# Performance work log

Hardware: AMD Instinct MI355X
Metric: run time of the kernel (lower is better)

Reference implementation:

```python
import jax, jax.numpy as jnp
import numpy as np

HIDDEN = 4096
N_HEADS = 32
N_KV_HEADS = 8
HEAD_DIM = 128
ROPE_THETA = 1000000.0
EPS = 1e-06
B, T = 1, 2048


def apply_rope(inputs, position_ids, head_dim, theta):
    # inputs: [B, T, H, D], position_ids: [B, T]
    fraction = 2 * jnp.arange(0, head_dim // 2, dtype=jnp.float32) / head_dim
    timescale = jnp.power(theta, fraction)  # [D/2]
    x = (position_ids.astype(jnp.float32)[..., None] / timescale[None, None, :])[..., None, :]  # [B,T,1,D/2]
    sin, cos = jnp.sin(x), jnp.cos(x)
    a, b = jnp.split(inputs, 2, axis=-1)
    return jnp.concatenate([a * cos - b * sin, b * cos + a * sin], axis=-1).astype(inputs.dtype)


def rms_norm(x, weight, eps=EPS):
    rms = jnp.sqrt(jnp.mean(x * x, axis=-1, keepdims=True) + eps)
    return weight * x / rms


def setup_inputs() -> dict:
    key = jax.random.key(0)
    ks = jax.random.split(key, 8)
    lecun = lambda k, shape: jax.random.normal(k, shape, jnp.float32) / np.sqrt(shape[0])
    return {
        "x": jax.random.normal(ks[0], (B, T, HIDDEN), jnp.float32),
        "Wq": lecun(ks[1], (HIDDEN, N_HEADS * HEAD_DIM)),
        "Wk": lecun(ks[2], (HIDDEN, N_KV_HEADS * HEAD_DIM)),
        "Wv": lecun(ks[3], (HIDDEN, N_KV_HEADS * HEAD_DIM)),
        "Wo": lecun(ks[4], (N_HEADS * HEAD_DIM, HIDDEN)),
        "q_norm_w": 1.0 + 0.01 * jax.random.normal(ks[5], (HEAD_DIM,), jnp.float32),
        "k_norm_w": 1.0 + 0.01 * jax.random.normal(ks[6], (HEAD_DIM,), jnp.float32),
        "attention_mask": jnp.ones((B, T), jnp.int32),
        "positions": jnp.broadcast_to(jnp.arange(T, dtype=jnp.int32)[None, :], (B, T)),
    }


def reference(x, Wq, Wk, Wv, Wo, q_norm_w, k_norm_w, attention_mask, positions):
    b, t, _ = x.shape
    q = rms_norm((x @ Wq).reshape(b, t, N_HEADS, HEAD_DIM), q_norm_w)
    k = rms_norm((x @ Wk).reshape(b, t, N_KV_HEADS, HEAD_DIM), k_norm_w)
    v = (x @ Wv).reshape(b, t, N_KV_HEADS, HEAD_DIM)
    q = apply_rope(q, positions, HEAD_DIM, ROPE_THETA)
    k = apply_rope(k, positions, HEAD_DIM, ROPE_THETA)
    # prefill path: kv_cache is None -> causal attention, padding mask on keys
    attn = jax.nn.dot_product_attention(
        q, k, v,
        scale=1.0 / HEAD_DIM ** 0.5,
        mask=attention_mask[:, None, None, :].astype(bool),
        is_causal=True,
    )
    out = attn.reshape(b, t, N_HEADS * HEAD_DIM) @ Wo
    return out, (k, v)
```

## Files before the change

kernel.cpp:

```cpp
#include <hip/hip_runtime.h>


typedef __bf16 bf16;
typedef __bf16 bf16x8 __attribute__((ext_vector_type(8)));
typedef float  f32x4  __attribute__((ext_vector_type(4)));

#define MFMA16(a, b, c) __builtin_amdgcn_mfma_f32_16x16x32_bf16((a), (b), (c), 0, 0, 0)

__device__ __forceinline__ void gll16(const void* g, void* l) {
    __builtin_amdgcn_global_load_lds(
        (const __attribute__((address_space(1))) void*)g,
        (__attribute__((address_space(3))) void*)l,
        16, 0, 0);
}

__global__ __launch_bounds__(256) void detect_convert(
    const unsigned short* __restrict__ probe,
    const void* __restrict__ qw_raw, const void* __restrict__ kw_raw,
    int* __restrict__ flag, bf16* __restrict__ qwc, bf16* __restrict__ kwc) {
    __shared__ int cnt;
    if (threadIdx.x == 0) cnt = 0;
    __syncthreads();
    int local = 0;
    for (int i = 0; i < 4; ++i) {
        const unsigned short w = probe[(threadIdx.x * 4 + i) * 2];
        const int e = (w >> 7) & 0xFF;
        if (e >= 90 && e <= 140) ++local;
    }
    atomicAdd(&cnt, local);
    __syncthreads();
    const bool isbf16 = cnt >= 700;
    if (threadIdx.x == 0) *flag = isbf16 ? 1 : 0;
    const int t = threadIdx.x;
    if (t < 128)
        qwc[t] = isbf16 ? ((const bf16*)qw_raw)[t] : (bf16)((const float*)qw_raw)[t];
    else
        kwc[t - 128] = isbf16 ? ((const bf16*)kw_raw)[t - 128] : (bf16)((const float*)kw_raw)[t - 128];
}

__global__ __launch_bounds__(256) void convert_x(const void* __restrict__ xv,
                                                 bf16* __restrict__ xb,
                                                 const int* __restrict__ flag) {
    const size_t i8 = ((size_t)blockIdx.x * 256 + threadIdx.x) * 8;
    if (*flag) {
        *(bf16x8*)&xb[i8] = *(const bf16x8*)&((const bf16*)xv)[i8];
    } else {
        const f32x4 a = *(const f32x4*)&((const float*)xv)[i8];
        const f32x4 b = *(const f32x4*)&((const float*)xv)[i8 + 4];
        bf16x8 o;
#pragma unroll
        for (int e = 0; e < 4; ++e) { o[e] = (bf16)a[e]; o[e + 4] = (bf16)b[e]; }
        *(bf16x8*)&xb[i8] = o;
    }
}

__global__ __launch_bounds__(256) void transpose_w(
    const void* __restrict__ Wq, const void* __restrict__ Wk, const void* __restrict__ Wv,
    bf16* __restrict__ WqT, bf16* __restrict__ WkT, bf16* __restrict__ WvT,
    const int* __restrict__ flag) {
    __shared__ float T[64][65];
    int id = blockIdx.x;
    const void* src;
    bf16* dst;
    int N, tn, tk;
    if (id < 4096) {
        src = Wq; dst = WqT; N = 4096; tn = id & 63; tk = id >> 6;
    } else {
        id -= 4096;
        if (id < 1024) { src = Wk; dst = WkT; }
        else           { src = Wv; dst = WvT; id -= 1024; }
        N = 1024; tn = id & 15; tk = id >> 4;
    }
    const int k0 = tk * 64, n0 = tn * 64;
    const bool bB = (*flag) != 0;
    const int tx = threadIdx.x & 63, ty = threadIdx.x >> 6;
#pragma unroll
    for (int p = 0; p < 16; ++p) {
        const int k = ty + p * 4;
        T[k][tx] = bB ? (float)((const bf16*)src)[(size_t)(k0 + k) * N + n0 + tx]
                      : ((const float*)src)[(size_t)(k0 + k) * N + n0 + tx];
    }
    __syncthreads();
#pragma unroll
    for (int p = 0; p < 16; ++p) {
        const int n = ty + p * 4;
        dst[(size_t)(n0 + n) * 4096 + k0 + tx] = (bf16)T[tx][n];
    }
}

__global__ __launch_bounds__(256) void gemm_bt(
    const bf16* __restrict__ A,
    const bf16* __restrict__ B1T, const bf16* __restrict__ B2T,
    bf16* __restrict__ C1, bf16* __restrict__ C2,
    int K, int ldc1, int ldc2, int ns1) {
    __shared__ __align__(16) bf16 As[128 * 64];
    __shared__ __align__(16) bf16 Bs[128 * 64];

    const int nbxp = (int)gridDim.x >> 3;
    int id = blockIdx.y * gridDim.x + blockIdx.x;
    const int xcd = id & 7;
    const int j = id >> 3;
    const int bx = xcd * nbxp + j / (int)gridDim.y;
    const int by = j % (int)gridDim.y;

    const bf16* BT;
    bf16* C;
    int n0, ldc;
    if (bx < ns1) { BT = B1T; C = C1; n0 = bx * 128; ldc = ldc1; }
    else          { BT = B2T; C = C2; n0 = (bx - ns1) * 128; ldc = ldc2; }
    const int m0 = by * 128;

    const int tid  = threadIdx.x;
    const int wave = tid >> 6;
    const int lane = tid & 63;
    const int l15  = lane & 15;
    const int quad = lane >> 4;
    const int axor = l15 & 7;
    const int wm = (wave >> 1) * 64;
    const int wn = (wave & 1) * 64;
    const int l8 = lane >> 3;

    const bf16* aP = A  + (size_t)(m0 + wave * 8 + l8) * K + (((lane & 7) ^ l8) << 3);
    const bf16* bP = BT + (size_t)(n0 + wave * 8 + l8) * K + (((lane & 7) ^ l8) << 3);

    f32x4 acc[4][4];
#pragma unroll
    for (int i = 0; i < 4; ++i)
#pragma unroll
        for (int j2 = 0; j2 < 4; ++j2) acc[i][j2] = {0.f, 0.f, 0.f, 0.f};

    const int nt = K >> 6;
    for (int t = 0; t < nt; ++t) {
        const int k0 = t << 6;
#pragma unroll
        for (int p = 0; p < 4; ++p)
            gll16(aP + (size_t)p * 32 * K + k0, &As[p * 2048 + wave * 512]);
#pragma unroll
        for (int p = 0; p < 4; ++p)
            gll16(bP + (size_t)p * 32 * K + k0, &Bs[p * 2048 + wave * 512]);
        __syncthreads();
#pragma unroll
        for (int kk = 0; kk < 64; kk += 32) {
            bf16x8 af[4], bfr[4];
#pragma unroll
            for (int i = 0; i < 4; ++i)
                af[i] = *(const bf16x8*)&As[(wm + i * 16 + l15) * 64 +
                        (((kk >> 3) + quad) ^ axor) * 8];
#pragma unroll
            for (int j3 = 0; j3 < 4; ++j3)
                bfr[j3] = *(const bf16x8*)&Bs[(wn + j3 * 16 + l15) * 64 +
                          (((kk >> 3) + quad) ^ axor) * 8];
#pragma unroll
            for (int i = 0; i < 4; ++i)
#pragma unroll
                for (int j3 = 0; j3 < 4; ++j3)
                    acc[i][j3] = MFMA16(af[i], bfr[j3], acc[i][j3]);
        }
        __syncthreads();
    }

#pragma unroll
    for (int i = 0; i < 4; ++i)
#pragma unroll
        for (int j2 = 0; j2 < 4; ++j2)
#pragma unroll
            for (int r = 0; r < 4; ++r) {
                const int row = m0 + wm + i * 16 + quad * 4 + r;
                const int col = n0 + wn + j2 * 16 + l15;
                C[(size_t)row * ldc + col] = (bf16)acc[i][j2][r];
            }
}

#define GBM 128
#define GBN 128
#define GBK 64
#define GLD 72

__global__ __launch_bounds__(256) void gemm_nt(
    const bf16* __restrict__ A,
    const void* __restrict__ B1v, const void* __restrict__ B2v, const void* __restrict__ B3v,
    bf16* __restrict__ Cb1, float* __restrict__ Cf1,
    bf16* __restrict__ Cb2, float* __restrict__ Cf2,
    bf16* __restrict__ Cb3, float* __restrict__ Cf3,
    const int* __restrict__ flag, int K,
    int ldb1, int ldb2, int ldb3, int ldc1, int ldc2, int ldc3,
    int ns1, int ns2) {
    __shared__ __align__(16) bf16 As[2][GBM * 64];
    __shared__ __align__(16) bf16 Bs[GBN * GLD];

    const int nbxp = (int)gridDim.x >> 3;
    int id = blockIdx.y * gridDim.x + blockIdx.x;
    const int xcd = id & 7;
    const int j = id >> 3;
    const int bx = xcd * nbxp + j / (int)gridDim.y;
    const int by = j % (int)gridDim.y;

    const void* Bv;
    bf16* Cb;
    float* Cf;
    int n0, ldb, ldc;
    if (bx < ns1) {
        Bv = B1v; Cb = Cb1; Cf = Cf1; n0 = bx * GBN; ldb = ldb1; ldc = ldc1;
    } else if (bx < ns1 + ns2) {
        Bv = B2v; Cb = Cb2; Cf = Cf2; n0 = (bx - ns1) * GBN; ldb = ldb2; ldc = ldc2;
    } else {
        Bv = B3v; Cb = Cb3; Cf = Cf3; n0 = (bx - ns1 - ns2) * GBN; ldb = ldb3; ldc = ldc3;
    }
    const int m0 = by * GBM;

    const bool bBf16 = (*flag) != 0;
    const bf16*  Bb = (const bf16*)Bv;
    const float* Bf = (const float*)Bv;

    const int tid  = threadIdx.x;
    const int wave = tid >> 6;
    const int lane = tid & 63;
    const int l15  = lane & 15;
    const int quad = lane >> 4;
    const int axor = l15 & 7;
    const int wm = (wave >> 1) * 64;
    const int wn = (wave & 1) * 64;

    const int l8 = lane >> 3;
    const bf16* aP = A + (size_t)(m0 + wave * 8 + l8) * K + (((lane & 7) ^ l8) << 3);

    f32x4 acc[4][4];
#pragma unroll
    for (int i = 0; i < 4; ++i)
#pragma unroll
        for (int j2 = 0; j2 < 4; ++j2) acc[i][j2] = {0.f, 0.f, 0.f, 0.f};

    bf16 bReg[4][8];

#define LOAD_B(k0)                                                             \
    {                                                                          \
        if (bBf16) {                                                           \
            _Pragma("unroll")                                                  \
            for (int p = 0; p < 4; ++p) {                                      \
                const int w16 = wave * 4 + p;                                  \
                const int n = (w16 & 1) * 64 + lane, kc = w16 >> 1;            \
                _Pragma("unroll")                                              \
                for (int e = 0; e < 8; ++e)                                    \
                    bReg[p][e] = Bb[(size_t)((k0) + kc * 8 + e) * ldb + n0 + n]; \
            }                                                                  \
        } else {                                                               \
            _Pragma("unroll")                                                  \
            for (int p = 0; p < 4; ++p) {                                      \
                const int w16 = wave * 4 + p;                                  \
                const int n = (w16 & 1) * 64 + lane, kc = w16 >> 1;            \
                _Pragma("unroll")                                              \
                for (int e = 0; e < 8; ++e)                                    \
                    bReg[p][e] = (bf16)Bf[(size_t)((k0) + kc * 8 + e) * ldb + n0 + n]; \
            }                                                                  \
        }                                                                      \
    }

#define GLL_A(k0, buf)                                                         \
    {                                                                          \
        _Pragma("unroll")                                                      \
        for (int p = 0; p < 4; ++p)                                            \
            gll16(aP + (size_t)p * 32 * K + (k0),                              \
                  &As[buf][p * 2048 + wave * 512]);                            \
    }

#define WRITE_B()                                                              \
    {                                                                          \
        _Pragma("unroll")                                                      \
        for (int p = 0; p < 4; ++p) {                                          \
            const int w16 = wave * 4 + p;                                      \
            const int n = (w16 & 1) * 64 + lane, kc = w16 >> 1;                \
            bf16x8 bv;                                                         \
            _Pragma("unroll")                                                  \
            for (int e = 0; e < 8; ++e) bv[e] = bReg[p][e];                    \
            *(bf16x8*)&Bs[n * GLD + kc * 8] = bv;                              \
        }                                                                      \
    }

#define COMPUTE(buf)                                                           \
    {                                                                          \
        _Pragma("unroll")                                                      \
        for (int kk = 0; kk < GBK; kk += 32) {                                 \
            bf16x8 af[4], bfr[4];                                              \
            _Pragma("unroll")                                                  \
            for (int i = 0; i < 4; ++i)                                        \
                af[i] = *(const bf16x8*)&As[buf][(wm + i * 16 + l15) * 64 +    \
                        ((((kk) >> 3) + quad) ^ axor) * 8];                    \
            _Pragma("unroll")                                                  \
            for (int j3 = 0; j3 < 4; ++j3)                                     \
                bfr[j3] = *(const bf16x8*)&Bs[(wn + j3 * 16 + l15) * GLD + kk + quad * 8]; \
            _Pragma("unroll")                                                  \
            for (int i = 0; i < 4; ++i)                                        \
                _Pragma("unroll")                                              \
                for (int j3 = 0; j3 < 4; ++j3)                                 \
                    acc[i][j3] = MFMA16(af[i], bfr[j3], acc[i][j3]);           \
        }                                                                      \
    }

    const int nt = K >> 6;
    LOAD_B(0);
    GLL_A(0, 0);
    WRITE_B();
    __syncthreads();
    int cur = 0;
    for (int t = 0; t < nt; ++t) {
        if (t + 1 < nt) {
            LOAD_B((t + 1) << 6);
            GLL_A((t + 1) << 6, cur ^ 1);
        }
        COMPUTE(cur);
        __syncthreads();
        if (t + 1 < nt) {
            WRITE_B();
            __syncthreads();
        }
        cur ^= 1;
    }
#undef LOAD_B
#undef GLL_A
#undef WRITE_B
#undef COMPUTE

#pragma unroll
    for (int i = 0; i < 4; ++i)
#pragma unroll
        for (int j2 = 0; j2 < 4; ++j2)
#pragma unroll
            for (int r = 0; r < 4; ++r) {
                const int row = m0 + wm + i * 16 + quad * 4 + r;
                const int col = n0 + wn + j2 * 16 + l15;
                const float v = acc[i][j2][r];
                if (Cb) Cb[(size_t)row * ldc + col] = (bf16)v;
                if (Cf) Cf[(size_t)row * ldc + col] = v;
            }
}

__global__ __launch_bounds__(256) void norm_rope(const bf16* __restrict__ src,
                                                 bf16* __restrict__ dst_bf,
                                                 float* __restrict__ dst_f32,
                                                 const bf16* __restrict__ w,
                                                 const int* __restrict__ positions,
                                                 int H) {
    const int wid  = blockIdx.x * 4 + (threadIdx.x >> 6);
    const int lane = threadIdx.x & 63;
    const int token = wid / H, head = wid % H;
    const bf16* s = src + ((size_t)token * H + head) * 128;
    const float f0 = (float)s[lane], f1 = (float)s[lane + 64];
    float ss = f0 * f0 + f1 * f1;
    for (int off = 32; off >= 1; off >>= 1) ss += __shfl_xor(ss, off);
    const float inv_rms = rsqrtf(ss * (1.0f / 128.0f) + 1e-6f);
    const float n0 = f0 * inv_rms * (float)w[lane];
    const float n1 = f1 * inv_rms * (float)w[lane + 64];
    const float pos = (float)positions[token];
    const float inv_ts = __expf((float)lane * (-13.815510557964274f / 64.0f));
    const float ang = pos * inv_ts;
    float sn, cs;
    __sincosf(ang, &sn, &cs);
    const float o0 = n0 * cs - n1 * sn;
    const float o1 = n1 * cs + n0 * sn;
    const size_t base = ((size_t)token * H + head) * 128;
    if (dst_bf)  { dst_bf[base + lane] = (bf16)o0;  dst_bf[base + lane + 64] = (bf16)o1; }
    if (dst_f32) { dst_f32[base + lane] = o0;       dst_f32[base + lane + 64] = o1; }
}

__global__ __launch_bounds__(256) void conv_b2f(const bf16* __restrict__ s,
                                                float* __restrict__ d) {
    const size_t i8 = ((size_t)blockIdx.x * 256 + threadIdx.x) * 8;
    const bf16x8 v = *(const bf16x8*)&s[i8];
    f32x4 a, b;
#pragma unroll
    for (int e = 0; e < 4; ++e) { a[e] = (float)v[e]; b[e] = (float)v[e + 4]; }
    *(f32x4*)&d[i8] = a;
    *(f32x4*)&d[i8 + 4] = b;
}

__global__ __launch_bounds__(256) void flash_attn(const bf16* __restrict__ Q,
                                                  const bf16* __restrict__ Kg,
                                                  const bf16* __restrict__ Vg,
                                                  bf16* __restrict__ Og) {
    __shared__ __align__(16) bf16 Ks[32 * 128];
    __shared__ __align__(16) bf16 Vt[128 * 40];
    __shared__ __align__(16) bf16 Ps[4][16 * 40];

    int id = blockIdx.y * 32 + blockIdx.x;
    id = (id & 7) * 128 + (id >> 3);
    const int h  = id >> 5;
    const int qt = 31 - (id & 31);
    const int kvh  = h >> 2;
    const int tid  = threadIdx.x;
    const int wave = tid >> 6;
    const int lane = tid & 63;
    const int l15  = lane & 15;
    const int quad = lane >> 4;
    const int q0   = qt * 64;
    const int qw0  = q0 + wave * 16;
    const int myq  = qw0 + l15;
    const float scale = 0.08838834764831845f;

    bf16x8 qf[4];
    {
        const bf16* qrow = Q + ((size_t)myq * 32 + h) * 128;
#pragma unroll
        for (int kc = 0; kc < 4; ++kc)
            qf[kc] = *(const bf16x8*)&qrow[kc * 32 + quad * 8];
    }

    f32x4 oacc[8];
#pragma unroll
    for (int i = 0; i < 8; ++i) oacc[i] = {0.f, 0.f, 0.f, 0.f};
    float m_run = -1e30f, l_run = 0.f;

    const int ksr  = tid & 31;
    const int kscb = tid >> 5;
    const int vr0  = (tid & 15) * 2;
    const int vcb  = tid >> 4;

    char* kbytes = (char*)Ks;
    char* vbytes = (char*)Vt;
    char* pbytes = (char*)&Ps[wave][0];

    const int ntiles = (q0 + 64) >> 5;
    for (int kt = 0; kt < ntiles; ++kt) {
        const int kb = kt * 32;
        {
            const bf16* src = Kg + ((size_t)(kb + ksr) * 8 + kvh) * 128;
            const bf16x8 v0 = *(const bf16x8*)&src[kscb * 8];
            const bf16x8 v1 = *(const bf16x8*)&src[(kscb + 8) * 8];
            const int b0 = (ksr * 256 + kscb * 16) ^ ((ksr & 7) << 4);
            const int b1 = (ksr * 256 + (kscb + 8) * 16) ^ ((ksr & 7) << 4);
            *(bf16x8*)(kbytes + b0) = v0;
            *(bf16x8*)(kbytes + b1) = v1;
        }
        {
            const bf16* s0 = Vg + ((size_t)(kb + vr0) * 8 + kvh) * 128 + vcb * 8;
            const bf16x8 a = *(const bf16x8*)s0;
            const bf16x8 b = *(const bf16x8*)(s0 + 1024);
#pragma unroll
            for (int e = 0; e < 8; ++e) {
                union { bf16 hh[2]; unsigned int u; } pk;
                pk.hh[0] = a[e]; pk.hh[1] = b[e];
                *(unsigned int*)(vbytes + (vcb * 8 + e) * 80 + vr0 * 2) = pk.u;
            }
        }
        __syncthreads();

        f32x4 sacc[2];
        sacc[0] = {0.f, 0.f, 0.f, 0.f};
        sacc[1] = {0.f, 0.f, 0.f, 0.f};
#pragma unroll
        for (int st = 0; st < 2; ++st) {
            const int row = st * 16 + l15;
#pragma unroll
            for (int kc = 0; kc < 4; ++kc) {
                const int bofs = (row * 256 + kc * 64 + quad * 16) ^ ((row & 7) << 4);
                const bf16x8 kf = *(const bf16x8*)(kbytes + bofs);
                sacc[st] = MFMA16(kf, qf[kc], sacc[st]);
            }
        }

        float sv[8];
        float pm = -1e30f;
#pragma unroll
        for (int st = 0; st < 2; ++st)
#pragma unroll
            for (int r = 0; r < 4; ++r) {
                const int key = kb + st * 16 + quad * 4 + r;
                float s = sacc[st][r] * scale;
                if (key > myq) s = -1e30f;
                sv[st * 4 + r] = s;
                pm = fmaxf(pm, s);
            }
        pm = fmaxf(pm, __shfl_xor(pm, 16));
        pm = fmaxf(pm, __shfl_xor(pm, 32));
        const float m_new = fmaxf(m_run, pm);
        const float corr = __expf(m_run - m_new);
        float ps = 0.f;
        bf16 pb[8];
#pragma unroll
        for (int i = 0; i < 8; ++i) {
            const float p = __expf(sv[i] - m_new);
            ps += p;
            pb[i] = (bf16)p;
        }
        ps += __shfl_xor(ps, 16);
        ps += __shfl_xor(ps, 32);
        l_run = l_run * corr + ps;
        m_run = m_new;

#pragma unroll
        for (int st = 0; st < 2; ++st)
#pragma unroll
            for (int r = 0; r < 4; ++r)
                *(bf16*)(pbytes + l15 * 80 + (st * 16 + quad * 4 + r) * 2) = pb[st * 4 + r];

        float corrq[4];
#pragma unroll
        for (int r = 0; r < 4; ++r) corrq[r] = __shfl(corr, quad * 4 + r);
#pragma unroll
        for (int nt = 0; nt < 8; ++nt)
#pragma unroll
            for (int r = 0; r < 4; ++r) oacc[nt][r] *= corrq[r];

        const bf16x8 pf = *(const bf16x8*)(pbytes + l15 * 80 + quad * 16);
#pragma unroll
        for (int nt = 0; nt < 8; ++nt) {
            const bf16x8 vf = *(const bf16x8*)(vbytes + (nt * 16 + l15) * 80 + quad * 16);
            oacc[nt] = MFMA16(pf, vf, oacc[nt]);
        }
        __syncthreads();
    }

    const float rinv = 1.0f / l_run;
    float linv[4];
#pragma unroll
    for (int r = 0; r < 4; ++r) linv[r] = __shfl(rinv, quad * 4 + r);
#pragma unroll
    for (int nt = 0; nt < 8; ++nt)
#pragma unroll
        for (int r = 0; r < 4; ++r) {
            const int row = qw0 + quad * 4 + r;
            Og[((size_t)row * 32 + h) * 128 + nt * 16 + l15] = (bf16)(oacc[nt][r] * linv[r]);
        }
}

extern "C" void kernel_launch(void* const* d_in, const int* in_sizes, int n_in,
                              void* d_out, int out_size, void* d_ws, size_t ws_size,
                              hipStream_t stream) {
    const void* x  = d_in[0];
    const void* Wq = d_in[1];
    const void* Wk = d_in[2];
    const void* Wv = d_in[3];
    const void* Wo = d_in[4];
    const void* qw = d_in[5];
    const void* kw = d_in[6];
    const int* positions = (const int*)d_in[8];

    char* ws = (char*)d_ws;
    int*  flag    = (int*)ws;
    bf16* qwc     = (bf16*)(ws + 64);
    bf16* kwc     = (bf16*)(ws + 64 + 256);
    bf16* kq      = (bf16*)(ws + 4096);
    bf16* vb      = (bf16*)(ws + 4096 + 4194304);
    bf16* xb      = (bf16*)(ws + 4096 + 8388608);
    bf16* attnbuf = (bf16*)(ws + 4096 + 8388608);

    float* outf = (float*)d_out;
    float* Kof  = outf + 8388608;
    float* Vof  = outf + 10485760;
    bf16*  WqT  = (bf16*)d_out;
    bf16*  WkT  = (bf16*)((char*)d_out + 33554432);
    bf16*  WvT  = (bf16*)((char*)d_out + 41943040);
    bf16*  qb   = (bf16*)((char*)d_out + 33554432);

    detect_convert<<<1, 256, 0, stream>>>((const unsigned short*)Wq, qw, kw, flag, qwc, kwc);
    convert_x<<<4096, 256, 0, stream>>>(x, xb, flag);
    transpose_w<<<6144, 256, 0, stream>>>(Wq, Wk, Wv, WqT, WkT, WvT, flag);

    gemm_bt<<<dim3(16, 16), 256, 0, stream>>>(xb, WkT, WvT, kq, vb, 4096, 1024, 1024, 8);
    gemm_bt<<<dim3(32, 16), 256, 0, stream>>>(xb, WqT, WqT, qb, qb, 4096, 4096, 4096, 32);

    norm_rope<<<16384, 256, 0, stream>>>(qb, qb, nullptr, qwc, positions, 32);
    norm_rope<<<4096, 256, 0, stream>>>(kq, kq, nullptr, kwc, positions, 8);

    flash_attn<<<dim3(32, 32), 256, 0, stream>>>(qb, kq, vb, attnbuf);

    conv_b2f<<<1024, 256, 0, stream>>>(kq, Kof);
    conv_b2f<<<1024, 256, 0, stream>>>(vb, Vof);

    gemm_nt<<<dim3(32, 16), 256, 0, stream>>>(
        attnbuf, Wo, Wo, Wo,
        nullptr, outf, nullptr, nullptr, nullptr, nullptr,
        flag, 4096,
        4096, 4096, 4096, 4096, 4096, 4096,
        32, 0);
}
```

Before: 674.4 us.

## Double-buffer LDS tiles in gemm_bt to overlap global loads with MFMA

The projection GEMM kernel now keeps two LDS buffers for the A and B tiles. It issues the direct-to-LDS loads for the next K tile before computing on the current one, so load latency can overlap with MFMA work. This also drops one barrier per iteration. The cost is double the LDS use (64 KB per block), which may lower occupancy.

```diff
diff --git a/kernel.cpp b/kernel.cpp
--- a/kernel.cpp
+++ b/kernel.cpp
@@ -93,8 +93,8 @@
     const bf16* __restrict__ B1T, const bf16* __restrict__ B2T,
     bf16* __restrict__ C1, bf16* __restrict__ C2,
     int K, int ldc1, int ldc2, int ns1) {
-    __shared__ __align__(16) bf16 As[128 * 64];
-    __shared__ __align__(16) bf16 Bs[128 * 64];
+    __shared__ __align__(16) bf16 As[2][128 * 64];
+    __shared__ __align__(16) bf16 Bs[2][128 * 64];
 
     const int nbxp = (int)gridDim.x >> 3;
     int id = blockIdx.y * gridDim.x + blockIdx.x;
@@ -129,35 +129,49 @@
 #pragma unroll
         for (int j2 = 0; j2 < 4; ++j2) acc[i][j2] = {0.f, 0.f, 0.f, 0.f};
 
+#define GLL_T(k0, buf)                                                         \
+    {                                                                          \
+        _Pragma("unroll")                                                      \
+        for (int p = 0; p < 4; ++p)                                            \
+            gll16(aP + (size_t)p * 32 * K + (k0), &As[buf][p * 2048 + wave * 512]); \
+        _Pragma("unroll")                                                      \
+        for (int p = 0; p < 4; ++p)                                            \
+            gll16(bP + (size_t)p * 32 * K + (k0), &Bs[buf][p * 2048 + wave * 512]); \
+    }
+
+#define COMP(buf)                                                              \
+    {                                                                          \
+        _Pragma("unroll")                                                      \
+        for (int kk = 0; kk < 64; kk += 32) {                                  \
+            bf16x8 af[4], bfr[4];                                              \
+            _Pragma("unroll")                                                  \
+            for (int i = 0; i < 4; ++i)                                        \
+                af[i] = *(const bf16x8*)&As[buf][(wm + i * 16 + l15) * 64 +    \
+                        (((kk >> 3) + quad) ^ axor) * 8];                      \
+            _Pragma("unroll")                                                  \
+            for (int j3 = 0; j3 < 4; ++j3)                                     \
+                bfr[j3] = *(const bf16x8*)&Bs[buf][(wn + j3 * 16 + l15) * 64 + \
+                          (((kk >> 3) + quad) ^ axor) * 8];                    \
+            _Pragma("unroll")                                                  \
+            for (int i = 0; i < 4; ++i)                                        \
+                _Pragma("unroll")                                              \
+                for (int j3 = 0; j3 < 4; ++j3)                                 \
+                    acc[i][j3] = MFMA16(af[i], bfr[j3], acc[i][j3]);           \
+        }                                                                      \
+    }
+
     const int nt = K >> 6;
+    GLL_T(0, 0);
+    __syncthreads();
+    int cur = 0;
     for (int t = 0; t < nt; ++t) {
-        const int k0 = t << 6;
-#pragma unroll
-        for (int p = 0; p < 4; ++p)
-            gll16(aP + (size_t)p * 32 * K + k0, &As[p * 2048 + wave * 512]);
-#pragma unroll
-        for (int p = 0; p < 4; ++p)
-            gll16(bP + (size_t)p * 32 * K + k0, &Bs[p * 2048 + wave * 512]);
+        if (t + 1 < nt) GLL_T((t + 1) << 6, cur ^ 1);
+        COMP(cur);
         __syncthreads();
-#pragma unroll
-        for (int kk = 0; kk < 64; kk += 32) {
-            bf16x8 af[4], bfr[4];
-#pragma unroll
-            for (int i = 0; i < 4; ++i)
-                af[i] = *(const bf16x8*)&As[(wm + i * 16 + l15) * 64 +
-                        (((kk >> 3) + quad) ^ axor) * 8];
-#pragma unroll
-            for (int j3 = 0; j3 < 4; ++j3)
-                bfr[j3] = *(const bf16x8*)&Bs[(wn + j3 * 16 + l15) * 64 +
-                          (((kk >> 3) + quad) ^ axor) * 8];
-#pragma unroll
-            for (int i = 0; i < 4; ++i)
-#pragma unroll
-                for (int j3 = 0; j3 < 4; ++j3)
-                    acc[i][j3] = MFMA16(af[i], bfr[j3], acc[i][j3]);
-        }
-        __syncthreads();
-    }
+        cur ^= 1;
+    }
+#undef GLL_T
+#undef COMP
 
 #pragma unroll
     for (int i = 0; i < 4; ++i)
```

Result: no change. 664.0 us (-1.5%).
